# Optimization experiments

Hardware: AMD Instinct MI355X
Metric: run time of the kernel (lower is better)

Reference implementation:

```python
import jax, jax.numpy as jnp
import numpy as np

B, C, H, W = 1, 512, 24, 24
N_HEADS, WS = 8, 7
PAD = WS // 2
HEAD_DIM = C // N_HEADS


def setup_inputs() -> dict:
    key = jax.random.key(0)
    ks = jax.random.split(key, 7)
    s = 0.02
    return {
        "x": jax.random.normal(ks[0], (B, C, H, W), dtype=jnp.float32),
        "Wq": s * jax.random.normal(ks[1], (C, C), dtype=jnp.float32),
        "bq": s * jax.random.normal(ks[2], (C,), dtype=jnp.float32),
        "Wk": s * jax.random.normal(ks[3], (C, C), dtype=jnp.float32),
        "bk": s * jax.random.normal(ks[4], (C,), dtype=jnp.float32),
        "Wv": s * jax.random.normal(ks[5], (C, C), dtype=jnp.float32),
        "bv": s * jax.random.normal(ks[6], (C,), dtype=jnp.float32),
        # module initializes gamma to zero; use small nonzero so output depends on attention
        "gamma": jnp.full((1,), 0.1, dtype=jnp.float32),
    }


def _conv1x1(z, Wt, bt):
    # 1x1 Conv2d == per-pixel GEMM over channels
    return jnp.einsum("bchw,oc->bohw", z, Wt) + bt[None, :, None, None]


def _windows(z):
    # z: (B, C, H+ws-1, W+ws-1) -> (B, n_heads, head_dim, ws*ws*H*W)
    # matches torch unfold(2,ws,1).unfold(3,ws,1).permute(0,1,4,5,2,3).view(...)
    taps = [z[:, :, di:di + H, dj:dj + W] for di in range(WS) for dj in range(WS)]
    w = jnp.stack(taps, axis=2)  # (B, C, ws*ws, H, W)
    return w.reshape(B, N_HEADS, HEAD_DIM, WS * WS * H * W)


def reference(x, Wq, bq, Wk, bk, Wv, bv, gamma):
    q = _conv1x1(x, Wq, bq).reshape(B, N_HEADS, HEAD_DIM, H * W)  # (B,h,d,HW)
    xp = jnp.pad(x, ((0, 0), (0, 0), (PAD, PAD), (PAD, PAD)), mode="reflect")
    k = _windows(_conv1x1(xp, Wk, bk))  # (B,h,d,ws^2*HW)
    v = _windows(_conv1x1(xp, Wv, bv))  # (B,h,d,ws^2*HW)
    # NOTE: as written in the source, each query attends to ALL ws^2*H*W keys
    energy = jnp.einsum("bhdq,bhdk->bhqk", q, k)  # (B,h,HW,ws^2*HW)
    attn = jax.nn.softmax(energy, axis=-1)
    out_w = jnp.einsum("bhqk,bhdk->bhdq", attn, v).reshape(B, C, H, W)
    return gamma * out_w + x
```

## Files before the change

### kernel.cpp

```cpp
#include <hip/hip_runtime.h>

#define HW   576
#define CC   512
#define PW   30
#define PPK  1024
#define NS   4
#define SP   256

typedef float f32x4 __attribute__((ext_vector_type(4)));
typedef short s16x8 __attribute__((ext_vector_type(8)));

__device__ __forceinline__ unsigned short f2bf(float f) {
    unsigned u = __float_as_uint(f);
    return (unsigned short)((u + 0x7FFFu + ((u >> 16) & 1u)) >> 16);
}
__device__ __forceinline__ float bf2f(unsigned short h) {
    return __uint_as_float((unsigned)h << 16);
}

#define OFF_QT 0u
#define OFF_KT 589824u
#define OFF_VP 1638400u
#define OFF_MP 2686976u
#define OFF_LP 2760704u
#define OFF_OP 2834432u
#define OFF_XB 2834432u
#define OFF_WB 3424256u

__global__ __launch_bounds__(256) void cvt_bf16(
    const float* __restrict__ x, const float* __restrict__ Wq,
    const float* __restrict__ Wk, const float* __restrict__ Wv,
    unsigned short* __restrict__ xb, unsigned short* __restrict__ wb)
{
    const int b = blockIdx.x, t = threadIdx.x;
    if (b < 288) {
        const int i = (b * 256 + t) * 4;
        const float4 v = *(const float4*)&x[i];
        ushort4 o;
        o.x = f2bf(v.x); o.y = f2bf(v.y); o.z = f2bf(v.z); o.w = f2bf(v.w);
        *(ushort4*)&xb[i] = o;
    } else {
        const int wi = ((b - 288) * 256 + t) * 4;
        const int sel = wi >> 18;
        const int off = wi & 262143;
        const float* src = (sel == 0) ? Wq : (sel == 1) ? Wk : Wv;
        const float4 v = *(const float4*)&src[off];
        ushort4 o;
        o.x = f2bf(v.x); o.y = f2bf(v.y); o.z = f2bf(v.z); o.w = f2bf(v.w);
        *(ushort4*)&wb[wi] = o;
    }
}

__global__ __launch_bounds__(256) void qkv_mfma(
    const unsigned short* __restrict__ xb, const unsigned short* __restrict__ wb,
    const float* __restrict__ bq, const float* __restrict__ bk,
    const float* __restrict__ bv,
    unsigned short* __restrict__ qT, unsigned short* __restrict__ kT,
    unsigned short* __restrict__ vP)
{
    const int sel = blockIdx.z;
    const int bx = blockIdx.x, by = blockIdx.y;
    if (sel == 0 && bx >= 9) return;
    const int big0 = bx * 64;
    const float* bias = (sel == 0) ? bq : (sel == 1) ? bk : bv;

    __shared__ __align__(16) unsigned short Wl[2][64 * 40];
    __shared__ __align__(16) unsigned short Xl[2][64 * 40];
    __shared__ int smap[64];

    const int t = threadIdx.x;
    if (t < 64) {
        int pp = big0 + t;
        int src;
        if (sel == 0) src = pp;
        else {
            if (pp >= 900) pp = 899;
            int y  = pp / PW, xw = pp - y * PW;
            int iy = y - 3;  iy = (iy < 0) ? -iy : (iy > 23 ? 46 - iy : iy);
            int ix = xw - 3; ix = (ix < 0) ? -ix : (ix > 23 ? 46 - ix : ix);
            src = iy * 24 + ix;
        }
        smap[t] = src;
    }
    __syncthreads();

    const int wrow = t >> 2, wk_ = (t & 3) * 8;
    const unsigned short* Wrow =
        wb + (size_t)sel * 262144 + (size_t)(by * 64 + wrow) * CC + wk_;
    const int px4 = (t & 15) * 4, k2 = (t >> 4) * 2;

    s16x8 wreg;
    unsigned short xreg[8];
    auto loadW = [&](int k0) { wreg = *(const s16x8*)(Wrow + k0); };
    auto loadX = [&](int k0) {
        const unsigned short* r0 = xb + (size_t)(k0 + k2) * HW;
        const unsigned short* r1 = r0 + HW;
        if (sel == 0) {
            *(ushort4*)&xreg[0] = *(const ushort4*)(r0 + big0 + px4);
            *(ushort4*)&xreg[4] = *(const ushort4*)(r1 + big0 + px4);
        } else {
            #pragma unroll
            for (int i = 0; i < 4; ++i) {
                const int s = smap[px4 + i];
                xreg[i]     = r0[s];
                xreg[4 + i] = r1[s];
            }
        }
    };
    auto commit = [&](int bi) {
        *(s16x8*)&Wl[bi][wrow * 40 + wk_] = wreg;
        #pragma unroll
        for (int i = 0; i < 4; ++i) {
            unsigned u = (unsigned)xreg[i] | ((unsigned)xreg[4 + i] << 16);
            *(unsigned*)&Xl[bi][(px4 + i) * 40 + k2] = u;
        }
    };

    loadW(0);  loadX(0);
    commit(0);
    loadW(32); loadX(32);

    f32x4 acc[2][2];
    #pragma unroll
    for (int i = 0; i < 2; ++i)
        #pragma unroll
        for (int j = 0; j < 2; ++j) acc[i][j] = (f32x4){0.f, 0.f, 0.f, 0.f};

    const int lane = t & 63, wv = t >> 6;
    const int wm = (wv >> 1) * 32, wn = (wv & 1) * 32;
    const int fr = lane & 15, fq = lane >> 4;

    const unsigned short* Abase = (sel == 2) ? &Wl[0][0] : &Xl[0][0];
    const unsigned short* Bbase = (sel == 2) ? &Xl[0][0] : &Wl[0][0];

    __syncthreads();
    for (int it = 0; it < 16; ++it) {
        const int cur = it & 1;
        if (it < 15) commit(1 - cur);
        if (it < 14) { loadW((it + 2) * 32); loadX((it + 2) * 32); }
        const unsigned short* A = Abase + cur * 2560;
        const unsigned short* B = Bbase + cur * 2560;
        const s16x8 a0 = *(const s16x8*)&A[(wm +  0 + fr) * 40 + fq * 8];
        const s16x8 a1 = *(const s16x8*)&A[(wm + 16 + fr) * 40 + fq * 8];
        const s16x8 b0 = *(const s16x8*)&B[(wn +  0 + fr) * 40 + fq * 8];
        const s16x8 b1 = *(const s16x8*)&B[(wn + 16 + fr) * 40 + fq * 8];
        acc[0][0] = __builtin_amdgcn_mfma_f32_16x16x32_bf16(a0, b0, acc[0][0], 0, 0, 0);
        acc[0][1] = __builtin_amdgcn_mfma_f32_16x16x32_bf16(a0, b1, acc[0][1], 0, 0, 0);
        acc[1][0] = __builtin_amdgcn_mfma_f32_16x16x32_bf16(a1, b0, acc[1][0], 0, 0, 0);
        acc[1][1] = __builtin_amdgcn_mfma_f32_16x16x32_bf16(a1, b1, acc[1][1], 0, 0, 0);
        __syncthreads();
    }

    #pragma unroll
    for (int mi = 0; mi < 2; ++mi)
        #pragma unroll
        for (int ni = 0; ni < 2; ++ni)
            #pragma unroll
            for (int r = 0; r < 4; ++r) {
                const float vacc = acc[mi][ni][r];
                const int m = wm + mi * 16 + fq * 4 + r;
                const int n = wn + ni * 16 + fr;
                if (sel == 0) {
                    qT[((size_t)by * HW + big0 + m) * 64 + n] =
                        f2bf(vacc + bias[by * 64 + n]);
                } else if (sel == 1) {
                    const int p = big0 + m;
                    kT[((size_t)by * PPK + p) * 64 + n] =
                        (p < 900) ? f2bf(vacc + bias[by * 64 + n]) : (unsigned short)0;
                } else {
                    const int p = big0 + n;
                    vP[((size_t)by * 64 + m) * PPK + p] =
                        (p < 900) ? f2bf(vacc + bias[by * 64 + m]) : (unsigned short)0;
                }
            }
}

__global__ __launch_bounds__(256) void attn3(
    const unsigned short* __restrict__ qT, const unsigned short* __restrict__ kT,
    const unsigned short* __restrict__ vP, float* __restrict__ mP,
    float* __restrict__ lP, unsigned short* __restrict__ Op)
{
    const int q0 = blockIdx.x * 16;
    const int s  = blockIdx.y;
    const int hd = blockIdx.z;
    const int t  = threadIdx.x;
    const int lane = t & 63, w = t >> 6;
    const int fr = lane & 15, u = lane >> 4;

    __shared__ float cnt_s[SP];
    __shared__ __align__(16) unsigned short Wl[16 * 272];
    __shared__ float mw[64], lw[64];

    if (t < SP) {
        const int p = s * SP + t;
        float c = 0.f;
        if (p < 900) {
            const int y = p / PW, xw = p - y * PW;
            int cy = y + 1;  if (PW - y  < cy) cy = PW - y;  if (cy > 7) cy = 7;
            int cx = xw + 1; if (PW - xw < cx) cx = PW - xw; if (cx > 7) cx = 7;
            c = (float)(cy * cx);
        }
        cnt_s[t] = c;
    }

    const unsigned short* qrow = qT + ((size_t)hd * HW + q0 + fr) * 64 + u * 8;
    const s16x8 b0 = *(const s16x8*)qrow;
    const s16x8 b1 = *(const s16x8*)(qrow + 32);

    f32x4 e[4];
    #pragma unroll
    for (int t4 = 0; t4 < 4; ++t4) {
        const unsigned short* krow =
            kT + ((size_t)hd * PPK + s * SP + w * 64 + t4 * 16 + fr) * 64 + u * 8;
        const s16x8 a0 = *(const s16x8*)krow;
        const s16x8 a1 = *(const s16x8*)(krow + 32);
        f32x4 a = (f32x4){0.f, 0.f, 0.f, 0.f};
        a = __builtin_amdgcn_mfma_f32_16x16x32_bf16(a0, b0, a, 0, 0, 0);
        a = __builtin_amdgcn_mfma_f32_16x16x32_bf16(a1, b1, a, 0, 0, 0);
        e[t4] = a;
    }

    float m = -1e30f;
    #pragma unroll
    for (int t4 = 0; t4 < 4; ++t4)
        #pragma unroll
        for (int r = 0; r < 4; ++r) m = fmaxf(m, e[t4][r]);
    m = fmaxf(m, __shfl_xor(m, 16));
    m = fmaxf(m, __shfl_xor(m, 32));
    if (lane < 16) mw[w * 16 + lane] = m;
    __syncthreads();
    const float mq = fmaxf(fmaxf(mw[fr], mw[16 + fr]), fmaxf(mw[32 + fr], mw[48 + fr]));

    float sum = 0.f;
    #pragma unroll
    for (int t4 = 0; t4 < 4; ++t4) {
        unsigned short wb4[4];
        #pragma unroll
        for (int r = 0; r < 4; ++r) {
            const float wv2 = cnt_s[w * 64 + t4 * 16 + u * 4 + r] *
                              __expf(e[t4][r] - mq);
            sum += wv2;
            wb4[r] = f2bf(wv2);
        }
        const int ho = fr * 272 + w * 64 + t4 * 16 + u * 4;
        *(unsigned*)&Wl[ho]     = (unsigned)wb4[0] | ((unsigned)wb4[1] << 16);
        *(unsigned*)&Wl[ho + 2] = (unsigned)wb4[2] | ((unsigned)wb4[3] << 16);
    }
    sum += __shfl_xor(sum, 16);
    sum += __shfl_xor(sum, 32);
    if (lane < 16) lw[w * 16 + lane] = sum;
    __syncthreads();

    if (t < 16) {
        const float lq = lw[t] + lw[16 + t] + lw[32 + t] + lw[48 + t];
        const float mq2 = fmaxf(fmaxf(mw[t], mw[16 + t]),
                                fmaxf(mw[32 + t], mw[48 + t]));
        const int si = (hd * NS + s) * HW + q0 + t;
        lP[si] = lq;
        mP[si] = mq2;
    }

    f32x4 o = (f32x4){0.f, 0.f, 0.f, 0.f};
    const unsigned short* vrow =
        vP + ((size_t)hd * 64 + w * 16 + fr) * PPK + s * SP + u * 8;
    #pragma unroll
    for (int c = 0; c < 8; ++c) {
        const s16x8 aw = *(const s16x8*)&Wl[fr * 272 + c * 32 + u * 8];
        const s16x8 bv2 = *(const s16x8*)(vrow + c * 32);
        o = __builtin_amdgcn_mfma_f32_16x16x32_bf16(aw, bv2, o, 0, 0, 0);
    }
    #pragma unroll
    for (int r = 0; r < 4; ++r) {
        const size_t oi =
            ((size_t)(hd * NS + s) * HW + q0 + u * 4 + r) * 64 + w * 16 + fr;
        Op[oi] = f2bf(o[r]);
    }
}

__global__ __launch_bounds__(256) void combine(
    const unsigned short* __restrict__ Op, const float* __restrict__ mP,
    const float* __restrict__ lP, const float* __restrict__ x,
    const float* __restrict__ gamma, float* __restrict__ out)
{
    const int idx = blockIdx.x * 256 + threadIdx.x;
    const int c = idx / HW, q = idx - c * HW;
    const int hd = c >> 6, d = c & 63;
    const int sb = (hd * NS) * HW + q;
    const float m0 = mP[sb], m1 = mP[sb + HW], m2 = mP[sb + 2 * HW], m3 = mP[sb + 3 * HW];
    const float ms = fmaxf(fmaxf(m0, m1), fmaxf(m2, m3));
    const float a0 = __expf(m0 - ms), a1 = __expf(m1 - ms);
    const float a2 = __expf(m2 - ms), a3 = __expf(m3 - ms);
    const float l = lP[sb] * a0 + lP[sb + HW] * a1 +
                    lP[sb + 2 * HW] * a2 + lP[sb + 3 * HW] * a3;
    const float o =
        bf2f(Op[(size_t)(sb)          * 64 + d]) * a0 +
        bf2f(Op[(size_t)(sb + HW)     * 64 + d]) * a1 +
        bf2f(Op[(size_t)(sb + 2 * HW) * 64 + d]) * a2 +
        bf2f(Op[(size_t)(sb + 3 * HW) * 64 + d]) * a3;
    out[idx] = fmaf(gamma[0], o / l, x[idx]);
}

extern "C" void kernel_launch(void* const* d_in, const int* in_sizes, int n_in,
                              void* d_out, int out_size, void* d_ws, size_t ws_size,
                              hipStream_t stream) {
    const float* x     = (const float*)d_in[0];
    const float* Wq    = (const float*)d_in[1];
    const float* bq    = (const float*)d_in[2];
    const float* Wk    = (const float*)d_in[3];
    const float* bk    = (const float*)d_in[4];
    const float* Wv    = (const float*)d_in[5];
    const float* bv    = (const float*)d_in[6];
    const float* gamma = (const float*)d_in[7];
    float* out = (float*)d_out;

    char* wsb = (char*)d_ws;
    unsigned short* qT = (unsigned short*)(wsb + OFF_QT);
    unsigned short* kT = (unsigned short*)(wsb + OFF_KT);
    unsigned short* vP = (unsigned short*)(wsb + OFF_VP);
    float*          mP = (float*)(wsb + OFF_MP);
    float*          lP = (float*)(wsb + OFF_LP);
    unsigned short* Op = (unsigned short*)(wsb + OFF_OP);
    unsigned short* xb = (unsigned short*)(wsb + OFF_XB);
    unsigned short* wb = (unsigned short*)(wsb + OFF_WB);

    cvt_bf16<<<dim3(1056), 256, 0, stream>>>(x, Wq, Wk, Wv, xb, wb);
    qkv_mfma<<<dim3(16, 8, 3), 256, 0, stream>>>(xb, wb, bq, bk, bv, qT, kT, vP);
    attn3<<<dim3(36, NS, 8), 256, 0, stream>>>(qT, kT, vP, mP, lP, Op);
    combine<<<dim3(1152), 256, 0, stream>>>(Op, mP, lP, x, gamma, out);
}
```

Baseline: 109.2 us.

## Transpose x to pixel-major bf16 and compute QKV with direct-load per-wave MFMA

The bf16 conversion now transposes x into a pixel-major layout with a zero pad row. That lets a new QKV kernel load A/B fragments directly from global memory per wave, with no LDS staging or block syncs, and apply reflect-padding through an index function. The weight conversion handles 8 elements per thread, and the combine kernel is restructured so each thread handles 16 channels with vectorized Op loads. The aim is to cut launch and LDS overhead in the projection and raise memory efficiency in the combine step. The risk is uncached, redundant global reads in the GEMM and strided output stores in the combine.

```diff
diff --git a/kernel.cpp b/kernel.cpp
--- a/kernel.cpp
+++ b/kernel.cpp
@@ -17,6 +17,13 @@
 __device__ __forceinline__ float bf2f(unsigned short h) {
     return __uint_as_float((unsigned)h << 16);
 }
+__device__ __forceinline__ int smapf(int p) {
+    if (p >= 900) return 576;
+    const int y = p / PW, xw = p - y * PW;
+    int iy = y - 3;  iy = (iy < 0) ? -iy : (iy > 23 ? 46 - iy : iy);
+    int ix = xw - 3; ix = (ix < 0) ? -ix : (ix > 23 ? 46 - ix : ix);
+    return iy * 24 + ix;
+}
 
 #define OFF_QT 0u
 #define OFF_KT 589824u
@@ -24,155 +31,113 @@
 #define OFF_MP 2686976u
 #define OFF_LP 2760704u
 #define OFF_OP 2834432u
-#define OFF_XB 2834432u
-#define OFF_WB 3424256u
-
-__global__ __launch_bounds__(256) void cvt_bf16(
-    const float* __restrict__ x, const float* __restrict__ Wq,
-    const float* __restrict__ Wk, const float* __restrict__ Wv,
-    unsigned short* __restrict__ xb, unsigned short* __restrict__ wb)
+#define OFF_XT 5193728u
+#define OFF_WB 5784576u
+
+__global__ __launch_bounds__(256) void cvtT(
+    const float* __restrict__ x,
+    const float* __restrict__ Wq, const float* __restrict__ Wk,
+    const float* __restrict__ Wv,
+    unsigned short* __restrict__ xT, unsigned short* __restrict__ wb)
 {
     const int b = blockIdx.x, t = threadIdx.x;
-    if (b < 288) {
-        const int i = (b * 256 + t) * 4;
-        const float4 v = *(const float4*)&x[i];
-        ushort4 o;
-        o.x = f2bf(v.x); o.y = f2bf(v.y); o.z = f2bf(v.z); o.w = f2bf(v.w);
-        *(ushort4*)&xb[i] = o;
+    if (b < 72) {
+        __shared__ float tile[64][65];
+        const int pt = b % 9, ct = b / 9;
+        const int p0 = pt * 64, c0 = ct * 64;
+        const int tr = t >> 4, tc4 = (t & 15) * 4;
+        #pragma unroll
+        for (int cr = 0; cr < 4; ++cr) {
+            const int row = cr * 16 + tr;
+            const float4 v = *(const float4*)&x[(size_t)(c0 + row) * HW + p0 + tc4];
+            tile[row][tc4 + 0] = v.x;
+            tile[row][tc4 + 1] = v.y;
+            tile[row][tc4 + 2] = v.z;
+            tile[row][tc4 + 3] = v.w;
+        }
+        __syncthreads();
+        #pragma unroll
+        for (int cr = 0; cr < 4; ++cr) {
+            const int prow = cr * 16 + tr;
+            ushort4 o;
+            o.x = f2bf(tile[tc4 + 0][prow]);
+            o.y = f2bf(tile[tc4 + 1][prow]);
+            o.z = f2bf(tile[tc4 + 2][prow]);
+            o.w = f2bf(tile[tc4 + 3][prow]);
+            *(ushort4*)&xT[(size_t)(p0 + prow) * CC + c0 + tc4] = o;
+        }
+    } else if (b == 72) {
+        if (t < 128) *(ushort4*)&xT[(size_t)576 * CC + t * 4] = (ushort4){0, 0, 0, 0};
     } else {
-        const int wi = ((b - 288) * 256 + t) * 4;
-        const int sel = wi >> 18;
-        const int off = wi & 262143;
+        const int wi = (b - 73) * 2048 + t * 8;
+        const int sel = wi >> 18, off = wi & 262143;
         const float* src = (sel == 0) ? Wq : (sel == 1) ? Wk : Wv;
-        const float4 v = *(const float4*)&src[off];
-        ushort4 o;
-        o.x = f2bf(v.x); o.y = f2bf(v.y); o.z = f2bf(v.z); o.w = f2bf(v.w);
-        *(ushort4*)&wb[wi] = o;
-    }
-}
-
-__global__ __launch_bounds__(256) void qkv_mfma(
-    const unsigned short* __restrict__ xb, const unsigned short* __restrict__ wb,
+        const float4 v0 = *(const float4*)&src[off];
+        const float4 v1 = *(const float4*)&src[off + 4];
+        ushort4 o0, o1;
+        o0.x = f2bf(v0.x); o0.y = f2bf(v0.y); o0.z = f2bf(v0.z); o0.w = f2bf(v0.w);
+        o1.x = f2bf(v1.x); o1.y = f2bf(v1.y); o1.z = f2bf(v1.z); o1.w = f2bf(v1.w);
+        *(ushort4*)&wb[wi]     = o0;
+        *(ushort4*)&wb[wi + 4] = o1;
+    }
+}
+
+__global__ __launch_bounds__(256) void qkv_direct(
+    const unsigned short* __restrict__ xT, const unsigned short* __restrict__ wb,
     const float* __restrict__ bq, const float* __restrict__ bk,
     const float* __restrict__ bv,
     unsigned short* __restrict__ qT, unsigned short* __restrict__ kT,
     unsigned short* __restrict__ vP)
 {
-    const int sel = blockIdx.z;
-    const int bx = blockIdx.x, by = blockIdx.y;
-    if (sel == 0 && bx >= 9) return;
-    const int big0 = bx * 64;
-    const float* bias = (sel == 0) ? bq : (sel == 1) ? bk : bv;
-
-    __shared__ __align__(16) unsigned short Wl[2][64 * 40];
-    __shared__ __align__(16) unsigned short Xl[2][64 * 40];
-    __shared__ int smap[64];
-
     const int t = threadIdx.x;
-    if (t < 64) {
-        int pp = big0 + t;
-        int src;
-        if (sel == 0) src = pp;
-        else {
-            if (pp >= 900) pp = 899;
-            int y  = pp / PW, xw = pp - y * PW;
-            int iy = y - 3;  iy = (iy < 0) ? -iy : (iy > 23 ? 46 - iy : iy);
-            int ix = xw - 3; ix = (ix < 0) ? -ix : (ix > 23 ? 46 - ix : ix);
-            src = iy * 24 + ix;
-        }
-        smap[t] = src;
-    }
-    __syncthreads();
-
-    const int wrow = t >> 2, wk_ = (t & 3) * 8;
-    const unsigned short* Wrow =
-        wb + (size_t)sel * 262144 + (size_t)(by * 64 + wrow) * CC + wk_;
-    const int px4 = (t & 15) * 4, k2 = (t >> 4) * 2;
-
-    s16x8 wreg;
-    unsigned short xreg[8];
-    auto loadW = [&](int k0) { wreg = *(const s16x8*)(Wrow + k0); };
-    auto loadX = [&](int k0) {
-        const unsigned short* r0 = xb + (size_t)(k0 + k2) * HW;
-        const unsigned short* r1 = r0 + HW;
-        if (sel == 0) {
-            *(ushort4*)&xreg[0] = *(const ushort4*)(r0 + big0 + px4);
-            *(ushort4*)&xreg[4] = *(const ushort4*)(r1 + big0 + px4);
-        } else {
-            #pragma unroll
-            for (int i = 0; i < 4; ++i) {
-                const int s = smap[px4 + i];
-                xreg[i]     = r0[s];
-                xreg[4 + i] = r1[s];
+    const int w = blockIdx.x * 4 + (t >> 6);
+    const int lane = t & 63, fr = lane & 15, u = lane >> 4;
+
+    int sel, m0, n0;
+    if (w < 576)       { sel = 0; m0 = (w >> 4) << 4;               n0 = (w & 15) << 5; }
+    else if (w < 1600) { const int k = w - 576;  sel = 1; m0 = (k >> 4) << 4; n0 = (k & 15) << 5; }
+    else               { const int k = w - 1600; sel = 2; m0 = (k >> 5) << 4; n0 = (k & 31) << 5; }
+
+    const unsigned short *A, *B;
+    int ar, bn0, bn1;
+    if (sel == 0)      { A = xT;          B = wb;          ar = m0 + fr;
+                         bn0 = n0 + fr;          bn1 = n0 + 16 + fr; }
+    else if (sel == 1) { A = xT;          B = wb + 262144; ar = smapf(m0 + fr);
+                         bn0 = n0 + fr;          bn1 = n0 + 16 + fr; }
+    else               { A = wb + 524288; B = xT;          ar = m0 + fr;
+                         bn0 = smapf(n0 + fr);   bn1 = smapf(n0 + 16 + fr); }
+
+    const unsigned short* Ap  = A + (size_t)ar  * CC + u * 8;
+    const unsigned short* Bp0 = B + (size_t)bn0 * CC + u * 8;
+    const unsigned short* Bp1 = B + (size_t)bn1 * CC + u * 8;
+
+    f32x4 acc0 = (f32x4){0.f, 0.f, 0.f, 0.f};
+    f32x4 acc1 = (f32x4){0.f, 0.f, 0.f, 0.f};
+    #pragma unroll 8
+    for (int k0 = 0; k0 < CC; k0 += 32) {
+        const s16x8 a  = *(const s16x8*)(Ap  + k0);
+        const s16x8 b0 = *(const s16x8*)(Bp0 + k0);
+        const s16x8 b1 = *(const s16x8*)(Bp1 + k0);
+        acc0 = __builtin_amdgcn_mfma_f32_16x16x32_bf16(a, b0, acc0, 0, 0, 0);
+        acc1 = __builtin_amdgcn_mfma_f32_16x16x32_bf16(a, b1, acc1, 0, 0, 0);
+    }
+
+    #pragma unroll
+    for (int ni = 0; ni < 2; ++ni) {
+        const f32x4 acc = ni ? acc1 : acc0;
+        #pragma unroll
+        for (int r = 0; r < 4; ++r) {
+            const int m = m0 + u * 4 + r;
+            const int n = n0 + ni * 16 + fr;
+            if (sel == 0) {
+                qT[((size_t)(n >> 6) * HW + m) * 64 + (n & 63)] = f2bf(acc[r] + bq[n]);
+            } else if (sel == 1) {
+                kT[((size_t)(n >> 6) * PPK + m) * 64 + (n & 63)] = f2bf(acc[r] + bk[n]);
+            } else {
+                vP[((size_t)(m >> 6) * 64 + (m & 63)) * PPK + n] = f2bf(acc[r] + bv[m]);
             }
         }
-    };
-    auto commit = [&](int bi) {
-        *(s16x8*)&Wl[bi][wrow * 40 + wk_] = wreg;
-        #pragma unroll
-        for (int i = 0; i < 4; ++i) {
-            unsigned u = (unsigned)xreg[i] | ((unsigned)xreg[4 + i] << 16);
-            *(unsigned*)&Xl[bi][(px4 + i) * 40 + k2] = u;
-        }
-    };
-
-    loadW(0);  loadX(0);
-    commit(0);
-    loadW(32); loadX(32);
-
-    f32x4 acc[2][2];
-    #pragma unroll
-    for (int i = 0; i < 2; ++i)
-        #pragma unroll
-        for (int j = 0; j < 2; ++j) acc[i][j] = (f32x4){0.f, 0.f, 0.f, 0.f};
-
-    const int lane = t & 63, wv = t >> 6;
-    const int wm = (wv >> 1) * 32, wn = (wv & 1) * 32;
-    const int fr = lane & 15, fq = lane >> 4;
-
-    const unsigned short* Abase = (sel == 2) ? &Wl[0][0] : &Xl[0][0];
-    const unsigned short* Bbase = (sel == 2) ? &Xl[0][0] : &Wl[0][0];
-
-    __syncthreads();
-    for (int it = 0; it < 16; ++it) {
-        const int cur = it & 1;
-        if (it < 15) commit(1 - cur);
-        if (it < 14) { loadW((it + 2) * 32); loadX((it + 2) * 32); }
-        const unsigned short* A = Abase + cur * 2560;
-        const unsigned short* B = Bbase + cur * 2560;
-        const s16x8 a0 = *(const s16x8*)&A[(wm +  0 + fr) * 40 + fq * 8];
-        const s16x8 a1 = *(const s16x8*)&A[(wm + 16 + fr) * 40 + fq * 8];
-        const s16x8 b0 = *(const s16x8*)&B[(wn +  0 + fr) * 40 + fq * 8];
-        const s16x8 b1 = *(const s16x8*)&B[(wn + 16 + fr) * 40 + fq * 8];
-        acc[0][0] = __builtin_amdgcn_mfma_f32_16x16x32_bf16(a0, b0, acc[0][0], 0, 0, 0);
-        acc[0][1] = __builtin_amdgcn_mfma_f32_16x16x32_bf16(a0, b1, acc[0][1], 0, 0, 0);
-        acc[1][0] = __builtin_amdgcn_mfma_f32_16x16x32_bf16(a1, b0, acc[1][0], 0, 0, 0);
-        acc[1][1] = __builtin_amdgcn_mfma_f32_16x16x32_bf16(a1, b1, acc[1][1], 0, 0, 0);
-        __syncthreads();
-    }
-
-    #pragma unroll
-    for (int mi = 0; mi < 2; ++mi)
-        #pragma unroll
-        for (int ni = 0; ni < 2; ++ni)
-            #pragma unroll
-            for (int r = 0; r < 4; ++r) {
-                const float vacc = acc[mi][ni][r];
-                const int m = wm + mi * 16 + fq * 4 + r;
-                const int n = wn + ni * 16 + fr;
-                if (sel == 0) {
-                    qT[((size_t)by * HW + big0 + m) * 64 + n] =
-                        f2bf(vacc + bias[by * 64 + n]);
-                } else if (sel == 1) {
-                    const int p = big0 + m;
-                    kT[((size_t)by * PPK + p) * 64 + n] =
-                        (p < 900) ? f2bf(vacc + bias[by * 64 + n]) : (unsigned short)0;
-                } else {
-                    const int p = big0 + n;
-                    vP[((size_t)by * 64 + m) * PPK + p] =
-                        (p < 900) ? f2bf(vacc + bias[by * 64 + m]) : (unsigned short)0;
-                }
-            }
+    }
 }
 
 __global__ __launch_bounds__(256) void attn3(
@@ -277,27 +242,43 @@
     }
 }
 
-__global__ __launch_bounds__(256) void combine(
+__global__ __launch_bounds__(256) void combine2(
     const unsigned short* __restrict__ Op, const float* __restrict__ mP,
     const float* __restrict__ lP, const float* __restrict__ x,
     const float* __restrict__ gamma, float* __restrict__ out)
 {
-    const int idx = blockIdx.x * 256 + threadIdx.x;
-    const int c = idx / HW, q = idx - c * HW;
-    const int hd = c >> 6, d = c & 63;
+    const int hd = blockIdx.y;
+    const int q  = blockIdx.x * 64 + (threadIdx.x >> 2);
+    const int dq = (threadIdx.x & 3) * 16;
+
     const int sb = (hd * NS) * HW + q;
-    const float m0 = mP[sb], m1 = mP[sb + HW], m2 = mP[sb + 2 * HW], m3 = mP[sb + 3 * HW];
+    const float m0 = mP[sb], m1 = mP[sb + HW];
+    const float m2 = mP[sb + 2 * HW], m3 = mP[sb + 3 * HW];
     const float ms = fmaxf(fmaxf(m0, m1), fmaxf(m2, m3));
-    const float a0 = __expf(m0 - ms), a1 = __expf(m1 - ms);
-    const float a2 = __expf(m2 - ms), a3 = __expf(m3 - ms);
-    const float l = lP[sb] * a0 + lP[sb + HW] * a1 +
-                    lP[sb + 2 * HW] * a2 + lP[sb + 3 * HW] * a3;
-    const float o =
-        bf2f(Op[(size_t)(sb)          * 64 + d]) * a0 +
-        bf2f(Op[(size_t)(sb + HW)     * 64 + d]) * a1 +
-        bf2f(Op[(size_t)(sb + 2 * HW) * 64 + d]) * a2 +
-        bf2f(Op[(size_t)(sb + 3 * HW) * 64 + d]) * a3;
-    out[idx] = fmaf(gamma[0], o / l, x[idx]);
+    const float a[NS] = {__expf(m0 - ms), __expf(m1 - ms),
+                         __expf(m2 - ms), __expf(m3 - ms)};
+    const float l = lP[sb] * a[0] + lP[sb + HW] * a[1] +
+                    lP[sb + 2 * HW] * a[2] + lP[sb + 3 * HW] * a[3];
+    const float scale = gamma[0] / l;
+
+    float o[16] = {};
+    #pragma unroll
+    for (int s = 0; s < NS; ++s) {
+        const unsigned short* op = &Op[((size_t)(sb + s * HW)) * 64 + dq];
+        const uint4 u0 = *(const uint4*)op;
+        const uint4 u1 = *(const uint4*)(op + 8);
+        const unsigned uu[8] = {u0.x, u0.y, u0.z, u0.w, u1.x, u1.y, u1.z, u1.w};
+        #pragma unroll
+        for (int j = 0; j < 8; ++j) {
+            o[2 * j]     = fmaf(a[s], bf2f((unsigned short)(uu[j] & 0xFFFF)), o[2 * j]);
+            o[2 * j + 1] = fmaf(a[s], bf2f((unsigned short)(uu[j] >> 16)),    o[2 * j + 1]);
+        }
+    }
+    #pragma unroll
+    for (int i = 0; i < 16; ++i) {
+        const size_t gi = (size_t)(hd * 64 + dq + i) * HW + q;
+        out[gi] = fmaf(scale, o[i], x[gi]);
+    }
 }
 
 extern "C" void kernel_launch(void* const* d_in, const int* in_sizes, int n_in,
@@ -320,11 +301,11 @@
     float*          mP = (float*)(wsb + OFF_MP);
     float*          lP = (float*)(wsb + OFF_LP);
     unsigned short* Op = (unsigned short*)(wsb + OFF_OP);
-    unsigned short* xb = (unsigned short*)(wsb + OFF_XB);
+    unsigned short* xT = (unsigned short*)(wsb + OFF_XT);
     unsigned short* wb = (unsigned short*)(wsb + OFF_WB);
 
-    cvt_bf16<<<dim3(1056), 256, 0, stream>>>(x, Wq, Wk, Wv, xb, wb);
-    qkv_mfma<<<dim3(16, 8, 3), 256, 0, stream>>>(xb, wb, bq, bk, bv, qT, kT, vP);
+    cvtT<<<dim3(457), 256, 0, stream>>>(x, Wq, Wk, Wv, xT, wb);
+    qkv_direct<<<dim3(656), 256, 0, stream>>>(xT, wb, bq, bk, bv, qT, kT, vP);
     attn3<<<dim3(36, NS, 8), 256, 0, stream>>>(qT, kT, vP, mP, lP, Op);
-    combine<<<dim3(1152), 256, 0, stream>>>(Op, mP, lP, x, gamma, out);
-}
+    combine2<<<dim3(9, 8), 256, 0, stream>>>(Op, mP, lP, x, gamma, out);
+}
```

After: 107.8 us. No clear change (-1.2%).
